# Kernel optimization log

Hardware: AMD Instinct MI355X
Metric: run time of the kernel (lower is better)

The kernel has to match this reference:

```python
import jax, jax.numpy as jnp
import numpy as np
from jax import lax

NH = 8  # heads
BN_EPS = 1e-3


def setup_inputs() -> dict:
    key = jax.random.key(0)
    ks = jax.random.split(key, 8)
    B, C1, H, W = 8, 256, 64, 64
    N, GC, EC = 32, 512, 256
    return {
        "x": jax.random.normal(ks[0], (B, C1, H, W), jnp.float32),
        "guide": jax.random.normal(ks[1], (B, N, GC), jnp.float32),
        "gl_w": jax.random.normal(ks[2], (EC, GC), jnp.float32) * 0.02,
        "gl_b": jax.random.normal(ks[3], (EC,), jnp.float32) * 0.02,
        "attn_bias": jnp.zeros((NH,), jnp.float32),
        "proj_w": jax.random.normal(ks[4], (C1, C1, 3, 3), jnp.float32) * 0.02,
        "bn_gamma": jnp.ones((C1,), jnp.float32),
        "bn_beta": jnp.zeros((C1,), jnp.float32),
        "bn_mean": jax.random.normal(ks[5], (C1,), jnp.float32) * 0.1,
        "bn_var": jax.random.uniform(ks[6], (C1,), jnp.float32, 0.5, 1.5),
    }


def reference(x, guide, gl_w, gl_b, attn_bias, proj_w, bn_gamma, bn_beta, bn_mean, bn_var):
    bs, c1, h, w = x.shape
    hc = c1 // NH
    # guide projection: (B,N,gc) -> (B,N,ec) -> (B,N,nh,hc)
    g = jnp.einsum('bng,eg->bne', guide, gl_w) + gl_b
    g = g.reshape(bs, -1, NH, hc)
    # embed = x (c1 == ec, so no embedding conv)
    emb = x.reshape(bs, NH, hc, h, w)
    # guided scores, max over guides
    aw = jnp.einsum('bmchw,bnmc->bmhwn', emb, g).max(-1)  # (B,nh,H,W)
    aw = jax.nn.sigmoid(aw / jnp.sqrt(jnp.float32(hc)) + attn_bias[None, :, None, None])
    # proj conv: 3x3, stride 1, pad 1, no bias, then BN (eval mode), no act
    p = lax.conv_general_dilated(x, proj_w, (1, 1), ((1, 1), (1, 1)),
                                 dimension_numbers=('NCHW', 'OIHW', 'NCHW'))
    inv = bn_gamma / jnp.sqrt(bn_var + BN_EPS)
    p = p * inv[None, :, None, None] + (bn_beta - bn_mean * inv)[None, :, None, None]
    out = p.reshape(bs, NH, -1, h, w) * aw[:, :, None]
    return out.reshape(bs, -1, h, w)
```

## Files before the change

kernel.cpp:

```cpp
#include <hip/hip_runtime.h>

typedef unsigned short u16;
typedef unsigned int u32;
typedef __bf16 bf16x8 __attribute__((ext_vector_type(8)));
typedef float f32x4 __attribute__((ext_vector_type(4)));

#define OFF_G      0x000000
#define OFF_AW     0x040000
#define OFF_WT     0x140000
#define OFF_SHIFT  0x260000
#define OFF_XPAD   0x2F0000
#define XPAD_BYTES (8u*66u*66u*256u*2u)
#define WS_NEED    ((size_t)OFF_XPAD + (size_t)XPAD_BYTES)

__device__ __forceinline__ u16 f2bf(float f) {
  union { float f; u32 u; } v; v.f = f;
  return (u16)((v.u + 0x7FFFu + ((v.u >> 16) & 1u)) >> 16);
}

__device__ __forceinline__ void gl2lds16(const u16* g, u16* l) {
  __builtin_amdgcn_global_load_lds(
      (const __attribute__((address_space(1))) void*)g,
      (__attribute__((address_space(3))) void*)l, 16, 0, 0);
}

__device__ __forceinline__ bf16x8 cvt8(const float* p) {
  const float4 a = *(const float4*)p;
  const float4 b = *(const float4*)(p + 4);
  u16 t[8];
  t[0] = f2bf(a.x); t[1] = f2bf(a.y); t[2] = f2bf(a.z); t[3] = f2bf(a.w);
  t[4] = f2bf(b.x); t[5] = f2bf(b.y); t[6] = f2bf(b.z); t[7] = f2bf(b.w);
  return *(const bf16x8*)t;
}

__global__ __launch_bounds__(256) void g2_k(
    const float* __restrict__ w, const float* __restrict__ gamma,
    const float* __restrict__ beta, const float* __restrict__ mean,
    const float* __restrict__ var, u16* __restrict__ wt, float* __restrict__ shift,
    const float* __restrict__ guide, const float* __restrict__ glw,
    const float* __restrict__ glb, float* __restrict__ g) {
  const int tid = threadIdx.x;
  if (blockIdx.x < 256) {
    const int co = blockIdx.x;
    const float inv = gamma[co] / sqrtf(var[co] + 1e-3f);
    float v[9];
#pragma unroll
    for (int t = 0; t < 9; ++t) v[t] = w[(size_t)co * 2304 + tid * 9 + t];
#pragma unroll
    for (int t = 0; t < 9; ++t) wt[co * 2304 + t * 256 + tid] = f2bf(v[t] * inv);
    if (tid == 0) shift[co] = beta[co] - mean[co] * inv;
    return;
  }
  const int bid = blockIdx.x - 256;
  const int b  = bid >> 2;
  const int e0 = (bid & 3) * 64;
  const int lane = tid & 63;
  const int wn   = tid >> 6;
  const int l15  = lane & 15;
  const int kq   = lane >> 4;

  const float* ga0 = guide + (size_t)b * 16384 + (size_t)l15 * 512 + kq * 8;
  const float* gb0 = glw + (size_t)(e0 + wn * 16 + l15) * 512 + kq * 8;

  f32x4 acc[2];
  acc[0] = (f32x4){0.f, 0.f, 0.f, 0.f};
  acc[1] = (f32x4){0.f, 0.f, 0.f, 0.f};
#pragma unroll
  for (int kc = 0; kc < 16; ++kc) {
    const int k0 = kc * 32;
    const bf16x8 bfr = cvt8(gb0 + k0);
#pragma unroll
    for (int mi = 0; mi < 2; ++mi) {
      const bf16x8 af = cvt8(ga0 + (size_t)mi * 16 * 512 + k0);
      acc[mi] = __builtin_amdgcn_mfma_f32_16x16x32_bf16(af, bfr, acc[mi], 0, 0, 0);
    }
  }
  const int e = e0 + wn * 16 + l15;
  const float bv = glb[e];
#pragma unroll
  for (int mi = 0; mi < 2; ++mi)
#pragma unroll
    for (int j = 0; j < 4; ++j) {
      const int n = mi * 16 + kq * 4 + j;
      g[(size_t)b * 8192 + n * 256 + e] = acc[mi][j] + bv;
    }
}

__global__ __launch_bounds__(256) void xpaw2_k(const float* __restrict__ x,
                                               const float* __restrict__ g,
                                               const float* __restrict__ bias,
                                               u16* __restrict__ xp,
                                               float* __restrict__ aw) {
  __shared__ u16 tile[256][64];
  __shared__ u16 xT[64][256];
  const int tid = threadIdx.x;
  const int b = blockIdx.x >> 6, y = blockIdx.x & 63;
  const int lane = tid & 63;
  const int wv   = tid >> 6;
  const int l15  = lane & 15;
  const int kq   = lane >> 4;

  bf16x8 af[2][2];
#pragma unroll
  for (int rep = 0; rep < 2; ++rep) {
    const int m = wv + rep * 4;
#pragma unroll
    for (int mi2 = 0; mi2 < 2; ++mi2)
      af[rep][mi2] = cvt8(g + (size_t)b * 8192 + (mi2 * 16 + l15) * 256 + m * 32 + kq * 8);
  }

  {
    const int cb = tid >> 4, xq = tid & 15;
#pragma unroll
    for (int i = 0; i < 16; ++i) {
      const int c = i * 16 + cb;
      const float4 v = *(const float4*)(x + (size_t)(b * 256 + c) * 4096 + y * 64 + xq * 4);
      ushort4 o; o.x = f2bf(v.x); o.y = f2bf(v.y); o.z = f2bf(v.z); o.w = f2bf(v.w);
      *(ushort4*)(&tile[c][xq * 4]) = o;
    }
  }
  __syncthreads();

  const int px = tid & 63, cg = tid >> 6;
  {
    u32 wbuf[32];
#pragma unroll
    for (int j = 0; j < 32; ++j) {
      const u16 lo = tile[cg * 64 + 2 * j][px];
      const u16 hi = tile[cg * 64 + 2 * j + 1][px];
      wbuf[j] = (u32)lo | ((u32)hi << 16);
    }
    u16* dst = xp + ((size_t)(b * 66 + y + 1) * 66 + px + 1) * 256 + cg * 64;
#pragma unroll
    for (int q = 0; q < 8; ++q) {
      uint4 v; v.x = wbuf[q * 4]; v.y = wbuf[q * 4 + 1]; v.z = wbuf[q * 4 + 2]; v.w = wbuf[q * 4 + 3];
      *(uint4*)(dst + q * 8) = v;
      const int slot = (cg * 8 + q) ^ (px & 7);
      *(uint4*)(&xT[px][slot * 8]) = v;
    }
  }
  {
    uint4* rowbase = (uint4*)(xp + (size_t)(b * 66 + y + 1) * 66 * 256);
    if (tid < 32) rowbase[tid] = (uint4){0, 0, 0, 0};
    else if (tid < 64) rowbase[65 * 32 + (tid - 32)] = (uint4){0, 0, 0, 0};
    if (y == 0) {
      uint4* r0 = (uint4*)(xp + (size_t)(b * 66) * 66 * 256);
      for (int i = tid; i < 2112; i += 256) r0[i] = (uint4){0, 0, 0, 0};
    }
    if (y == 63) {
      uint4* r65 = (uint4*)(xp + (size_t)(b * 66 + 65) * 66 * 256);
      for (int i = tid; i < 2112; i += 256) r65[i] = (uint4){0, 0, 0, 0};
    }
  }
  __syncthreads();

#pragma unroll
  for (int rep = 0; rep < 2; ++rep) {
    const int m = wv + rep * 4;
    bf16x8 bfr[4];
#pragma unroll
    for (int ni2 = 0; ni2 < 4; ++ni2) {
      const int row = ni2 * 16 + l15;
      const int slot = (m * 4 + kq) ^ (row & 7);
      bfr[ni2] = *(const bf16x8*)(&xT[row][slot * 8]);
    }
    f32x4 acc[2][4];
#pragma unroll
    for (int i = 0; i < 2; ++i)
#pragma unroll
      for (int j = 0; j < 4; ++j) acc[i][j] = (f32x4){0.f, 0.f, 0.f, 0.f};
#pragma unroll
    for (int mi2 = 0; mi2 < 2; ++mi2)
#pragma unroll
      for (int ni2 = 0; ni2 < 4; ++ni2)
        acc[mi2][ni2] = __builtin_amdgcn_mfma_f32_16x16x32_bf16(af[rep][mi2], bfr[ni2], acc[mi2][ni2], 0, 0, 0);

    const float bm = bias[m];
#pragma unroll
    for (int ni2 = 0; ni2 < 4; ++ni2) {
      float v = acc[0][ni2][0];
#pragma unroll
      for (int j = 1; j < 4; ++j) v = fmaxf(v, acc[0][ni2][j]);
#pragma unroll
      for (int j = 0; j < 4; ++j) v = fmaxf(v, acc[1][ni2][j]);
      v = fmaxf(v, __shfl_xor(v, 16));
      v = fmaxf(v, __shfl_xor(v, 32));
      const float z = v * 0.17677669529663687f + bm;
      const float a = 1.f / (1.f + expf(-z));
      if (kq == 0)
        aw[(size_t)(b * 8 + m) * 4096 + y * 64 + ni2 * 16 + l15] = a;
    }
  }
}

__global__ void attnw_k(const float* __restrict__ x, const float* __restrict__ g,
                        const float* __restrict__ bias, float* __restrict__ aw) {
  const int bm = blockIdx.x;
  const int b = bm >> 3, m = bm & 7;
  const int p = blockIdx.y * 256 + threadIdx.x;
  const float* xp = x + (size_t)(b * 256 + m * 32) * 4096 + p;
  float xv[32];
#pragma unroll
  for (int c = 0; c < 32; ++c) xv[c] = xp[(size_t)c * 4096];
  const float* gv = g + b * 8192 + m * 32;
  float best = -3.4e38f;
#pragma unroll 4
  for (int n = 0; n < 32; ++n) {
    const float* grow = gv + n * 256;
    float s = 0.f;
#pragma unroll
    for (int c = 0; c < 32; ++c) s = fmaf(xv[c], grow[c], s);
    best = fmaxf(best, s);
  }
  const float z = best * 0.17677669529663687f + bias[m];
  aw[(size_t)bm * 4096 + p] = 1.f / (1.f + expf(-z));
}

#define A_U16 8192
#define B_U16 16384
#define BUF_U16 24576

#define STAGE8(koff, bof, ab, bb) do {                                     \
    _Pragma("unroll")                                                      \
    for (int q_ = 0; q_ < 2; ++q_)                                         \
      gl2lds16(awt + (size_t)q_ * 147456 + (koff), (ab) + wv * 512 + q_ * 4096); \
    _Pragma("unroll")                                                      \
    for (int q_ = 0; q_ < 4; ++q_)                                         \
      gl2lds16(bxt + (ptrdiff_t)q_ * 16896 + (bof), (bb) + wv * 512 + q_ * 4096); \
  } while (0)

__global__ __launch_bounds__(512) void conv8c_k(
    const u16* __restrict__ xp, const u16* __restrict__ wt,
    const float* __restrict__ shift, const float* __restrict__ aw,
    float* __restrict__ out) {
  __shared__ u16 lds[3 * BUF_U16];

  const int tid  = threadIdx.x;
  const int lane = tid & 63;
  const int wv   = tid >> 6;
  const int wm   = wv >> 2;
  const int wn   = wv & 3;

  const int pxt = blockIdx.x;
  const int co0 = blockIdx.y * 128;
  const int p0  = pxt * 256;
  const int b   = pxt >> 4;
  const int y0  = (pxt & 15) * 4;

  const int sr    = tid >> 3;
  const int sslot = (tid & 7) ^ (sr & 7);
  const u16* awt = wt + (size_t)(co0 + sr) * 2304 + sslot * 8;
  const u16* bxt = xp + ((size_t)(b * 66 + y0 + 1) * 66 + sr + 1) * 256 + sslot * 8;

  u16* aR  = lds;              u16* bR  = lds + A_U16;
  u16* aN1 = lds + BUF_U16;    u16* bN1 = lds + BUF_U16 + A_U16;
  u16* aN2 = lds + 2*BUF_U16;  u16* bN2 = lds + 2*BUF_U16 + A_U16;

  const int l15 = lane & 15;
  const int sx  = lane & 7;
  const int kq  = lane >> 4;
  const int aRowB = (wm * 64 + l15) * 128;
  const int bRowB = (wn * 64 + l15) * 128;

  f32x4 acc[4][4];
#pragma unroll
  for (int i = 0; i < 4; ++i)
#pragma unroll
    for (int j = 0; j < 4; ++j) acc[i][j] = (f32x4){0.f, 0.f, 0.f, 0.f};

  STAGE8(0,  -17152,      aR,  bR);
  STAGE8(64, -17152 + 64, aN1, bN1);

  int kbase = 0;
  for (int t = 0; t < 9; ++t) {
    const int bof_c = ((t / 3 - 1) * 66 + (t % 3 - 1)) * 256;
    const int t1 = t + 1;
    const int bof_n = (t1 < 9) ? ((t1 / 3 - 1) * 66 + (t1 % 3 - 1)) * 256 : 0;
#pragma unroll
    for (int q = 0; q < 4; ++q) {
      if (t == 8 && q == 3) {
        asm volatile("s_waitcnt vmcnt(0)" ::: "memory");
      } else {
        asm volatile("s_waitcnt vmcnt(6)" ::: "memory");
      }
      __builtin_amdgcn_s_barrier();
      __builtin_amdgcn_sched_barrier(0);

      if ((t < 8) || (q < 2)) {
        const int ksoff = kbase + (q + 2) * 64;
        const int bsoff = (q < 2) ? (bof_c + (q + 2) * 64) : (bof_n + (q - 2) * 64);
        STAGE8(ksoff, bsoff, aN2, bN2);
      }

      const char* Ac = (const char*)aR;
      const char* Bc = (const char*)bR;
#pragma unroll
      for (int ks = 0; ks < 2; ++ks) {
        const int slotb = ((((ks << 2) | kq) ^ sx) << 4);
        bf16x8 af[4], bfr[4];
#pragma unroll
        for (int mi = 0; mi < 4; ++mi)
          af[mi] = *(const bf16x8*)(Ac + aRowB + mi * 2048 + slotb);
#pragma unroll
        for (int ni = 0; ni < 4; ++ni)
          bfr[ni] = *(const bf16x8*)(Bc + bRowB + ni * 2048 + slotb);
        __builtin_amdgcn_s_setprio(1);
#pragma unroll
        for (int mi = 0; mi < 4; ++mi)
#pragma unroll
          for (int ni = 0; ni < 4; ++ni)
            acc[mi][ni] = __builtin_amdgcn_mfma_f32_16x16x32_bf16(af[mi], bfr[ni], acc[mi][ni], 0, 0, 0);
        __builtin_amdgcn_s_setprio(0);
      }

      __builtin_amdgcn_sched_barrier(0);
      __builtin_amdgcn_s_barrier();

      u16* ta = aR; aR = aN1; aN1 = aN2; aN2 = ta;
      u16* tb = bR; bR = bN1; bN1 = bN2; bN2 = tb;
    }
    kbase += 256;
  }

  const int pybase = p0 & 4095;
#pragma unroll
  for (int mi = 0; mi < 4; ++mi) {
#pragma unroll
    for (int j = 0; j < 4; ++j) {
      const int co = co0 + wm * 64 + mi * 16 + ((lane >> 4) << 2) + j;
      const float sh = shift[co];
      const float* awrow = aw + (size_t)(b * 8 + (co >> 5)) * 4096 + pybase;
      float* orow = out + (size_t)(b * 256 + co) * 4096 + pybase;
#pragma unroll
      for (int ni = 0; ni < 4; ++ni) {
        const int pp = wn * 64 + ni * 16 + l15;
        orow[pp] = (acc[mi][ni][j] + sh) * awrow[pp];
      }
    }
  }
}

#define LDK 72
__global__ __launch_bounds__(256) void conv_fb(
    const float* __restrict__ xf, const u16* __restrict__ wt,
    const float* __restrict__ shift, const float* __restrict__ aw,
    float* __restrict__ out) {
  __shared__ u16 As[128 * LDK];
  __shared__ u16 Bs[128 * LDK];
  const int tid  = threadIdx.x;
  const int lane = tid & 63;
  const int wave = tid >> 6;
  const int wm = wave >> 1, wn = wave & 1;
  const int p0  = blockIdx.x * 128;
  const int co0 = blockIdx.y * 128;
  const int b   = p0 >> 12;
  const int y0  = (p0 >> 6) & 63;
  const int bn   = tid & 127;
  const int half = tid >> 7;
  const int py = y0 + (bn >> 6);
  const int px = bn & 63;
  const long xbase = (long)b * (256L * 4096L);
  const int arow0 = tid >> 3;
  const int akc   = tid & 7;

  f32x4 acc[4][4];
#pragma unroll
  for (int i = 0; i < 4; ++i)
#pragma unroll
    for (int j = 0; j < 4; ++j) acc[i][j] = (f32x4){0.f, 0.f, 0.f, 0.f};

  for (int t = 0; t < 9; ++t) {
    const int dy = t / 3 - 1, dxx = t % 3 - 1;
    const int yy = py + dy, xg = px + dxx;
    const bool valid = ((unsigned)yy < 64u) && ((unsigned)xg < 64u);
    const long pixoff = xbase + (long)yy * 64 + xg;
    for (int ci0 = 0; ci0 < 256; ci0 += 64) {
      const int kbase = t * 256 + ci0;
#pragma unroll
      for (int q = 0; q < 4; ++q) {
        const int row = arow0 + q * 32;
        const uint4 v = *(const uint4*)(wt + (size_t)(co0 + row) * 2304 + kbase + akc * 8);
        *(uint4*)(&As[row * LDK + akc * 8]) = v;
      }
      {
        u32 vals[16];
        const int chb = ci0 + half * 32;
#pragma unroll
        for (int jj = 0; jj < 16; ++jj) {
          const float lo = valid ? xf[pixoff + (long)(chb + jj * 2) * 4096] : 0.f;
          const float hi = valid ? xf[pixoff + (long)(chb + jj * 2 + 1) * 4096] : 0.f;
          vals[jj] = (u32)f2bf(lo) | ((u32)f2bf(hi) << 16);
        }
#pragma unroll
        for (int q = 0; q < 4; ++q) {
          uint4 v; v.x = vals[q*4]; v.y = vals[q*4+1]; v.z = vals[q*4+2]; v.w = vals[q*4+3];
          *(uint4*)(&Bs[bn * LDK + half * 32 + q * 8]) = v;
        }
      }
      __syncthreads();
#pragma unroll
      for (int ks = 0; ks < 2; ++ks) {
        const int coloff = ks * 32 + (lane >> 4) * 8;
        bf16x8 af[4], bfr[4];
#pragma unroll
        for (int mi = 0; mi < 4; ++mi)
          af[mi] = *(const bf16x8*)(&As[(wm * 64 + mi * 16 + (lane & 15)) * LDK + coloff]);
#pragma unroll
        for (int ni = 0; ni < 4; ++ni)
          bfr[ni] = *(const bf16x8*)(&Bs[(wn * 64 + ni * 16 + (lane & 15)) * LDK + coloff]);
#pragma unroll
        for (int mi = 0; mi < 4; ++mi)
#pragma unroll
          for (int ni = 0; ni < 4; ++ni)
            acc[mi][ni] = __builtin_amdgcn_mfma_f32_16x16x32_bf16(af[mi], bfr[ni], acc[mi][ni], 0, 0, 0);
      }
      __syncthreads();
    }
  }
  const int pybase = p0 & 4095;
#pragma unroll
  for (int mi = 0; mi < 4; ++mi) {
#pragma unroll
    for (int j = 0; j < 4; ++j) {
      const int co = co0 + wm * 64 + mi * 16 + ((lane >> 4) << 2) + j;
      const float sh = shift[co];
      const float* awrow = aw + (size_t)(b * 8 + (co >> 5)) * 4096 + pybase;
      float* orow = out + (size_t)(b * 256 + co) * 4096 + pybase;
#pragma unroll
      for (int ni = 0; ni < 4; ++ni) {
        const int pp = wn * 64 + ni * 16 + (lane & 15);
        orow[pp] = (acc[mi][ni][j] + sh) * awrow[pp];
      }
    }
  }
}

extern "C" void kernel_launch(void* const* d_in, const int* in_sizes, int n_in,
                              void* d_out, int out_size, void* d_ws, size_t ws_size,
                              hipStream_t stream) {
  (void)in_sizes; (void)n_in; (void)out_size;
  const float* x     = (const float*)d_in[0];
  const float* guide = (const float*)d_in[1];
  const float* glw   = (const float*)d_in[2];
  const float* glb   = (const float*)d_in[3];
  const float* bias  = (const float*)d_in[4];
  const float* pw    = (const float*)d_in[5];
  const float* gamma = (const float*)d_in[6];
  const float* beta  = (const float*)d_in[7];
  const float* mean  = (const float*)d_in[8];
  const float* var   = (const float*)d_in[9];
  float* out = (float*)d_out;

  char* ws = (char*)d_ws;
  float* g     = (float*)(ws + OFF_G);
  float* aw    = (float*)(ws + OFF_AW);
  u16*   wt    = (u16*)(ws + OFF_WT);
  float* shift = (float*)(ws + OFF_SHIFT);
  u16*   xpad  = (u16*)(ws + OFF_XPAD);
  const int usexp = (ws_size >= WS_NEED) ? 1 : 0;

  g2_k<<<dim3(288), dim3(256), 0, stream>>>(pw, gamma, beta, mean, var, wt, shift,
                                            guide, glw, glb, g);
  if (usexp) {
    xpaw2_k<<<dim3(512), dim3(256), 0, stream>>>(x, g, bias, xpad, aw);
    conv8c_k<<<dim3(128, 2), dim3(512), 0, stream>>>(xpad, wt, shift, aw, out);
  } else {
    attnw_k<<<dim3(64, 16), dim3(256), 0, stream>>>(x, g, bias, aw);
    conv_fb<<<dim3(256, 2), dim3(256), 0, stream>>>(x, wt, shift, aw, out);
  }
}
```

Baseline: 71.18 us.

## Split K across wave pairs in conv kernel with 1024-thread blocks and LDS reduction

```diff
diff --git a/kernel.cpp b/kernel.cpp
--- a/kernel.cpp
+++ b/kernel.cpp
@@ -220,16 +220,13 @@
 #define B_U16 16384
 #define BUF_U16 24576
 
-#define STAGE8(koff, bof, ab, bb) do {                                     \
-    _Pragma("unroll")                                                      \
-    for (int q_ = 0; q_ < 2; ++q_)                                         \
-      gl2lds16(awt + (size_t)q_ * 147456 + (koff), (ab) + wv * 512 + q_ * 4096); \
-    _Pragma("unroll")                                                      \
-    for (int q_ = 0; q_ < 4; ++q_)                                         \
-      gl2lds16(bxt + (ptrdiff_t)q_ * 16896 + (bof), (bb) + wv * 512 + q_ * 4096); \
+#define STAGE16(koff, bof, ab, bb) do {                                    \
+    gl2lds16(awt  + (koff), (ab) + wv * 512);                              \
+    gl2lds16(bxt0 + (bof),  (bb) + wv * 512);                              \
+    gl2lds16(bxt1 + (bof),  (bb) + 8192 + wv * 512);                       \
   } while (0)
 
-__global__ __launch_bounds__(512) void conv8c_k(
+__global__ __launch_bounds__(1024, 4) void conv16_k(
     const u16* __restrict__ xp, const u16* __restrict__ wt,
     const float* __restrict__ shift, const float* __restrict__ aw,
     float* __restrict__ out) {
@@ -238,8 +235,10 @@
   const int tid  = threadIdx.x;
   const int lane = tid & 63;
   const int wv   = tid >> 6;
-  const int wm   = wv >> 2;
-  const int wn   = wv & 3;
+  const int wks  = wv & 1;
+  const int wid2 = wv >> 1;
+  const int wm   = wid2 >> 2;
+  const int wn   = wid2 & 3;
 
   const int pxt = blockIdx.x;
   const int co0 = blockIdx.y * 128;
@@ -247,10 +246,11 @@
   const int b   = pxt >> 4;
   const int y0  = (pxt & 15) * 4;
 
-  const int sr    = tid >> 3;
-  const int sslot = (tid & 7) ^ (sr & 7);
-  const u16* awt = wt + (size_t)(co0 + sr) * 2304 + sslot * 8;
-  const u16* bxt = xp + ((size_t)(b * 66 + y0 + 1) * 66 + sr + 1) * 256 + sslot * 8;
+  const int srow = tid >> 3;
+  const int sl   = (tid & 7) ^ (srow & 7);
+  const u16* awt  = wt + (size_t)(co0 + srow) * 2304 + sl * 8;
+  const u16* bxt0 = xp + ((size_t)(b * 66 + y0 + (srow >> 6) + 1) * 66 + (srow & 63) + 1) * 256 + sl * 8;
+  const u16* bxt1 = bxt0 + 2 * 66 * 256;
 
   u16* aR  = lds;              u16* bR  = lds + A_U16;
   u16* aN1 = lds + BUF_U16;    u16* bN1 = lds + BUF_U16 + A_U16;
@@ -261,6 +261,7 @@
   const int kq  = lane >> 4;
   const int aRowB = (wm * 64 + l15) * 128;
   const int bRowB = (wn * 64 + l15) * 128;
+  const int slotb = (((wks << 2) | kq) ^ sx) << 4;
 
   f32x4 acc[4][4];
 #pragma unroll
@@ -268,8 +269,8 @@
 #pragma unroll
     for (int j = 0; j < 4; ++j) acc[i][j] = (f32x4){0.f, 0.f, 0.f, 0.f};
 
-  STAGE8(0,  -17152,      aR,  bR);
-  STAGE8(64, -17152 + 64, aN1, bN1);
+  STAGE16(0,  -17152,      aR,  bR);
+  STAGE16(64, -17152 + 64, aN1, bN1);
 
   int kbase = 0;
   for (int t = 0; t < 9; ++t) {
@@ -281,7 +282,7 @@
       if (t == 8 && q == 3) {
         asm volatile("s_waitcnt vmcnt(0)" ::: "memory");
       } else {
-        asm volatile("s_waitcnt vmcnt(6)" ::: "memory");
+        asm volatile("s_waitcnt vmcnt(3)" ::: "memory");
       }
       __builtin_amdgcn_s_barrier();
       __builtin_amdgcn_sched_barrier(0);
@@ -289,29 +290,25 @@
       if ((t < 8) || (q < 2)) {
         const int ksoff = kbase + (q + 2) * 64;
         const int bsoff = (q < 2) ? (bof_c + (q + 2) * 64) : (bof_n + (q - 2) * 64);
-        STAGE8(ksoff, bsoff, aN2, bN2);
+        STAGE16(ksoff, bsoff, aN2, bN2);
       }
 
       const char* Ac = (const char*)aR;
       const char* Bc = (const char*)bR;
-#pragma unroll
-      for (int ks = 0; ks < 2; ++ks) {
-        const int slotb = ((((ks << 2) | kq) ^ sx) << 4);
-        bf16x8 af[4], bfr[4];
-#pragma unroll
-        for (int mi = 0; mi < 4; ++mi)
-          af[mi] = *(const bf16x8*)(Ac + aRowB + mi * 2048 + slotb);
+      bf16x8 af[4], bfr[4];
+#pragma unroll
+      for (int mi = 0; mi < 4; ++mi)
+        af[mi] = *(const bf16x8*)(Ac + aRowB + mi * 2048 + slotb);
+#pragma unroll
+      for (int ni = 0; ni < 4; ++ni)
+        bfr[ni] = *(const bf16x8*)(Bc + bRowB + ni * 2048 + slotb);
+      __builtin_amdgcn_s_setprio(1);
+#pragma unroll
+      for (int mi = 0; mi < 4; ++mi)
 #pragma unroll
         for (int ni = 0; ni < 4; ++ni)
-          bfr[ni] = *(const bf16x8*)(Bc + bRowB + ni * 2048 + slotb);
-        __builtin_amdgcn_s_setprio(1);
-#pragma unroll
-        for (int mi = 0; mi < 4; ++mi)
-#pragma unroll
-          for (int ni = 0; ni < 4; ++ni)
-            acc[mi][ni] = __builtin_amdgcn_mfma_f32_16x16x32_bf16(af[mi], bfr[ni], acc[mi][ni], 0, 0, 0);
-        __builtin_amdgcn_s_setprio(0);
-      }
+          acc[mi][ni] = __builtin_amdgcn_mfma_f32_16x16x32_bf16(af[mi], bfr[ni], acc[mi][ni], 0, 0, 0);
+      __builtin_amdgcn_s_setprio(0);
 
       __builtin_amdgcn_sched_barrier(0);
       __builtin_amdgcn_s_barrier();
@@ -321,6 +318,25 @@
     }
     kbase += 256;
   }
+
+  float* red = (float*)lds;
+  if (wks) {
+#pragma unroll
+    for (int mi = 0; mi < 4; ++mi)
+#pragma unroll
+      for (int ni = 0; ni < 4; ++ni)
+        *(f32x4*)(red + (size_t)(wid2 * 16 + mi * 4 + ni) * 256 + lane * 4) = acc[mi][ni];
+  }
+  __syncthreads();
+  if (wks) return;
+
+#pragma unroll
+  for (int mi = 0; mi < 4; ++mi)
+#pragma unroll
+    for (int ni = 0; ni < 4; ++ni) {
+      const f32x4 o = *(const f32x4*)(red + (size_t)(wid2 * 16 + mi * 4 + ni) * 256 + lane * 4);
+      acc[mi][ni] += o;
+    }
 
   const int pybase = p0 & 4095;
 #pragma unroll
@@ -463,7 +479,7 @@
                                             guide, glw, glb, g);
   if (usexp) {
     xpaw2_k<<<dim3(512), dim3(256), 0, stream>>>(x, g, bias, xpad, aw);
-    conv8c_k<<<dim3(128, 2), dim3(512), 0, stream>>>(xpad, wt, shift, aw, out);
+    conv16_k<<<dim3(128, 2), dim3(1024), 0, stream>>>(xpad, wt, shift, aw, out);
   } else {
     attnw_k<<<dim3(64, 16), dim3(256), 0, stream>>>(x, g, bias, aw);
     conv_fb<<<dim3(256, 2), dim3(256), 0, stream>>>(x, wt, shift, aw, out);
```

New measurement: 72.64 us. +2.0%, slower.

## Load conv weight fragments directly into registers, keep only activations in LDS

Applied to the files above, without the earlier changes.

```diff
diff --git a/kernel.cpp b/kernel.cpp
--- a/kernel.cpp
+++ b/kernel.cpp
@@ -216,24 +216,28 @@
   aw[(size_t)bm * 4096 + p] = 1.f / (1.f + expf(-z));
 }
 
-#define A_U16 8192
 #define B_U16 16384
-#define BUF_U16 24576
-
-#define STAGE8(koff, bof, ab, bb) do {                                     \
-    _Pragma("unroll")                                                      \
-    for (int q_ = 0; q_ < 2; ++q_)                                         \
-      gl2lds16(awt + (size_t)q_ * 147456 + (koff), (ab) + wv * 512 + q_ * 4096); \
+
+#define STAGE_B(bof, bb) do {                                              \
     _Pragma("unroll")                                                      \
     for (int q_ = 0; q_ < 4; ++q_)                                         \
       gl2lds16(bxt + (ptrdiff_t)q_ * 16896 + (bof), (bb) + wv * 512 + q_ * 4096); \
   } while (0)
 
-__global__ __launch_bounds__(512) void conv8c_k(
+#define LOAD_A(koff, dst) do {                                             \
+    _Pragma("unroll")                                                      \
+    for (int mi_ = 0; mi_ < 4; ++mi_)                                      \
+      _Pragma("unroll")                                                    \
+      for (int ks_ = 0; ks_ < 2; ++ks_)                                    \
+        (dst)[mi_ * 2 + ks_] = *(const bf16x8*)(awt0 + (size_t)mi_ * 36864 \
+                                                + (koff) + ks_ * 32);      \
+  } while (0)
+
+__global__ __launch_bounds__(512, 2) void conv8e_k(
     const u16* __restrict__ xp, const u16* __restrict__ wt,
     const float* __restrict__ shift, const float* __restrict__ aw,
     float* __restrict__ out) {
-  __shared__ u16 lds[3 * BUF_U16];
+  __shared__ u16 lds[3 * B_U16];
 
   const int tid  = threadIdx.x;
   const int lane = tid & 63;
@@ -249,27 +253,29 @@
 
   const int sr    = tid >> 3;
   const int sslot = (tid & 7) ^ (sr & 7);
-  const u16* awt = wt + (size_t)(co0 + sr) * 2304 + sslot * 8;
   const u16* bxt = xp + ((size_t)(b * 66 + y0 + 1) * 66 + sr + 1) * 256 + sslot * 8;
-
-  u16* aR  = lds;              u16* bR  = lds + A_U16;
-  u16* aN1 = lds + BUF_U16;    u16* bN1 = lds + BUF_U16 + A_U16;
-  u16* aN2 = lds + 2*BUF_U16;  u16* bN2 = lds + 2*BUF_U16 + A_U16;
 
   const int l15 = lane & 15;
   const int sx  = lane & 7;
   const int kq  = lane >> 4;
-  const int aRowB = (wm * 64 + l15) * 128;
+  const u16* awt0 = wt + (size_t)(co0 + wm * 64 + l15) * 2304 + kq * 8;
   const int bRowB = (wn * 64 + l15) * 128;
 
+  u16* bR  = lds;
+  u16* bN1 = lds + B_U16;
+  u16* bN2 = lds + 2 * B_U16;
+
   f32x4 acc[4][4];
 #pragma unroll
   for (int i = 0; i < 4; ++i)
 #pragma unroll
     for (int j = 0; j < 4; ++j) acc[i][j] = (f32x4){0.f, 0.f, 0.f, 0.f};
 
-  STAGE8(0,  -17152,      aR,  bR);
-  STAGE8(64, -17152 + 64, aN1, bN1);
+  bf16x8 aA[8], aB[8];
+
+  STAGE_B(-17152,      bR);
+  STAGE_B(-17152 + 64, bN1);
+  LOAD_A(0, aA);
 
   int kbase = 0;
   for (int t = 0; t < 9; ++t) {
@@ -278,45 +284,54 @@
     const int bof_n = (t1 < 9) ? ((t1 / 3 - 1) * 66 + (t1 % 3 - 1)) * 256 : 0;
 #pragma unroll
     for (int q = 0; q < 4; ++q) {
-      if (t == 8 && q == 3) {
-        asm volatile("s_waitcnt vmcnt(0)" ::: "memory");
+      if (t == 0 && q == 0) {
+        asm volatile("s_waitcnt vmcnt(12)" ::: "memory");
+      } else if (t == 8 && q == 3) {
+        asm volatile("s_waitcnt vmcnt(16)" ::: "memory");
       } else {
-        asm volatile("s_waitcnt vmcnt(6)" ::: "memory");
+        asm volatile("s_waitcnt vmcnt(20)" ::: "memory");
       }
       __builtin_amdgcn_s_barrier();
       __builtin_amdgcn_sched_barrier(0);
 
       if ((t < 8) || (q < 2)) {
-        const int ksoff = kbase + (q + 2) * 64;
         const int bsoff = (q < 2) ? (bof_c + (q + 2) * 64) : (bof_n + (q - 2) * 64);
-        STAGE8(ksoff, bsoff, aN2, bN2);
-      }
-
-      const char* Ac = (const char*)aR;
+        STAGE_B(bsoff, bN2);
+      }
+      if ((t < 8) || (q < 3)) {
+        const int koff_n = (q < 3) ? (kbase + (q + 1) * 64) : (kbase + 256);
+        if ((q & 1) == 0) { LOAD_A(koff_n, aB); } else { LOAD_A(koff_n, aA); }
+      }
+      __builtin_amdgcn_sched_barrier(0);
+
       const char* Bc = (const char*)bR;
 #pragma unroll
       for (int ks = 0; ks < 2; ++ks) {
         const int slotb = ((((ks << 2) | kq) ^ sx) << 4);
-        bf16x8 af[4], bfr[4];
-#pragma unroll
-        for (int mi = 0; mi < 4; ++mi)
-          af[mi] = *(const bf16x8*)(Ac + aRowB + mi * 2048 + slotb);
+        bf16x8 bfr[4];
 #pragma unroll
         for (int ni = 0; ni < 4; ++ni)
           bfr[ni] = *(const bf16x8*)(Bc + bRowB + ni * 2048 + slotb);
         __builtin_amdgcn_s_setprio(1);
-#pragma unroll
-        for (int mi = 0; mi < 4; ++mi)
-#pragma unroll
-          for (int ni = 0; ni < 4; ++ni)
-            acc[mi][ni] = __builtin_amdgcn_mfma_f32_16x16x32_bf16(af[mi], bfr[ni], acc[mi][ni], 0, 0, 0);
+        if ((q & 1) == 0) {
+#pragma unroll
+          for (int mi = 0; mi < 4; ++mi)
+#pragma unroll
+            for (int ni = 0; ni < 4; ++ni)
+              acc[mi][ni] = __builtin_amdgcn_mfma_f32_16x16x32_bf16(aA[mi * 2 + ks], bfr[ni], acc[mi][ni], 0, 0, 0);
+        } else {
+#pragma unroll
+          for (int mi = 0; mi < 4; ++mi)
+#pragma unroll
+            for (int ni = 0; ni < 4; ++ni)
+              acc[mi][ni] = __builtin_amdgcn_mfma_f32_16x16x32_bf16(aB[mi * 2 + ks], bfr[ni], acc[mi][ni], 0, 0, 0);
+        }
         __builtin_amdgcn_s_setprio(0);
       }
 
       __builtin_amdgcn_sched_barrier(0);
       __builtin_amdgcn_s_barrier();
 
-      u16* ta = aR; aR = aN1; aN1 = aN2; aN2 = ta;
       u16* tb = bR; bR = bN1; bN1 = bN2; bN2 = tb;
     }
     kbase += 256;
@@ -463,7 +478,7 @@
                                             guide, glw, glb, g);
   if (usexp) {
     xpaw2_k<<<dim3(512), dim3(256), 0, stream>>>(x, g, bias, xpad, aw);
-    conv8c_k<<<dim3(128, 2), dim3(512), 0, stream>>>(xpad, wt, shift, aw, out);
+    conv8e_k<<<dim3(128, 2), dim3(512), 0, stream>>>(xpad, wt, shift, aw, out);
   } else {
     attnw_k<<<dim3(64, 16), dim3(256), 0, stream>>>(x, g, bias, aw);
     conv_fb<<<dim3(256, 2), dim3(256), 0, stream>>>(x, wt, shift, aw, out);
```

Measured after the change: 122.3 us. 1.72x slower.
